# Performance work log

Measured on AMD Instinct MI355X. Metric: run time of the kernel, lower is better.

## Reference

```python
import jax, jax.numpy as jnp
import numpy as np

DEPTH = 4
DIM = 1024
HEADS = 16
DIM_HEAD = 64
INNER = HEADS * DIM_HEAD  # 1024
MLP = 4096
CTX = 768
SCALE = DIM_HEAD ** -0.5
EPS = 1e-5


def setup_inputs() -> dict:
    key = jax.random.key(0)
    ks = jax.random.split(key, 12)
    def rn(k, shape, s=0.02):
        return jax.random.normal(k, shape, jnp.float32) * s
    return {
        "x": jax.random.normal(ks[0], (2, 2048, DIM), jnp.float32),
        "context": jax.random.normal(ks[1], (2, 1024, CTX), jnp.float32),
        "ln1_g": jnp.ones((DEPTH, DIM), jnp.float32),
        "ln1_b": jnp.zeros((DEPTH, DIM), jnp.float32),
        "w_qkv": rn(ks[2], (DEPTH, DIM, 3 * INNER)),
        "w_sa_o": rn(ks[3], (DEPTH, INNER, DIM)),
        "b_sa_o": jnp.zeros((DEPTH, DIM), jnp.float32),
        "ln2_g": jnp.ones((DEPTH, DIM), jnp.float32),
        "ln2_b": jnp.zeros((DEPTH, DIM), jnp.float32),
        "w_q": rn(ks[4], (DEPTH, DIM, INNER)),
        "w_kv": rn(ks[5], (DEPTH, CTX, 2 * INNER)),
        "w_ca_o": rn(ks[6], (DEPTH, INNER, DIM)),
        "b_ca_o": jnp.zeros((DEPTH, DIM), jnp.float32),
        "ln3_g": jnp.ones((DEPTH, DIM), jnp.float32),
        "ln3_b": jnp.zeros((DEPTH, DIM), jnp.float32),
        "w_ff1": rn(ks[7], (DEPTH, DIM, MLP)),
        "b_ff1": jnp.zeros((DEPTH, MLP), jnp.float32),
        "w_ff2": rn(ks[8], (DEPTH, MLP, DIM)),
        "b_ff2": jnp.zeros((DEPTH, DIM), jnp.float32),
    }


def _ln(x, g, b):
    mu = jnp.mean(x, axis=-1, keepdims=True)
    var = jnp.mean(jnp.square(x - mu), axis=-1, keepdims=True)
    return (x - mu) * jax.lax.rsqrt(var + EPS) * g + b


def _heads(t):
    # [b, n, h*d] -> [b, h, n, d]
    b, n, _ = t.shape
    return t.reshape(b, n, HEADS, DIM_HEAD).transpose(0, 2, 1, 3)


def _mha(q, k, v):
    # q,k,v: [b, h, n, d]; naive matmul-softmax-matmul, same math as the torch code
    attn = jax.nn.softmax(jnp.einsum('bhqd,bhkd->bhqk', q, k) * SCALE, axis=-1)
    out = jnp.einsum('bhqk,bhkd->bhqd', attn, v)
    b, h, n, d = out.shape
    return out.transpose(0, 2, 1, 3).reshape(b, n, h * d)


def reference(x, context, ln1_g, ln1_b, w_qkv, w_sa_o, b_sa_o,
              ln2_g, ln2_b, w_q, w_kv, w_ca_o, b_ca_o,
              ln3_g, ln3_b, w_ff1, b_ff1, w_ff2, b_ff2):
    for i in range(DEPTH):
        # self-attention
        h = _ln(x, ln1_g[i], ln1_b[i])
        qkv = h @ w_qkv[i]
        q, k, v = jnp.split(qkv, 3, axis=-1)
        sa = _mha(_heads(q), _heads(k), _heads(v)) @ w_sa_o[i] + b_sa_o[i]
        x = sa + x
        # cross-attention
        h = _ln(x, ln2_g[i], ln2_b[i])
        q = h @ w_q[i]
        kv = context @ w_kv[i]
        k, v = jnp.split(kv, 2, axis=-1)
        ca = _mha(_heads(q), _heads(k), _heads(v)) @ w_ca_o[i] + b_ca_o[i]
        x = ca + x
        # feed-forward (exact GELU, matching torch nn.GELU default)
        h = _ln(x, ln3_g[i], ln3_b[i])
        ff = jax.nn.gelu(h @ w_ff1[i] + b_ff1[i], approximate=False) @ w_ff2[i] + b_ff2[i]
        x = ff + x
    return x
```

## Files before the change

### kernel.cpp

```cpp
#include <hip/hip_runtime.h>
#include <hip/hip_bf16.h>
#include <math.h>

typedef __bf16 bf16_t;
typedef __bf16 bf16x8 __attribute__((ext_vector_type(8)));
typedef __bf16 bf16x4 __attribute__((ext_vector_type(4)));
typedef float f32x4 __attribute__((ext_vector_type(4)));
typedef unsigned short u16;
typedef unsigned int u32;
typedef u16 u16x8 __attribute__((ext_vector_type(8)));

#define NDEPTH 4
#define DIM 1024
#define NHEADS 16
#define MLP_DIM 4096
#define CTXD 768
#define NTOK 4096
#define NCTX 2048
#define ATT_SCALE 0.125f

__device__ inline void gload_lds16(const void* g, void* l) {
  __builtin_amdgcn_global_load_lds(
      (const __attribute__((address_space(1))) void*)g,
      (__attribute__((address_space(3))) void*)l, 16, 0, 0);
}

__device__ inline u32 packbf2(float a, float b) {
  union { bf16_t h[2]; u32 w; } u;
  u.h[0] = (bf16_t)a; u.h[1] = (bf16_t)b;
  return u.w;
}

template<int EPI>
__global__ __launch_bounds__(256) void gemm_bf16(
    const bf16_t* __restrict__ A, const bf16_t* __restrict__ Bt,
    const float* __restrict__ bias, const float* __restrict__ res,
    void* __restrict__ outp, int M, int N, int K)
{
  __shared__ bf16_t As[2][128 * 32];
  __shared__ bf16_t Bs[2][128 * 32];
  const int tid = threadIdx.x, lane = tid & 63, wave = tid >> 6;
  const int bx = blockIdx.x, by = blockIdx.y;
  const int wr = wave >> 1, wc = wave & 1;
  const int l15 = lane & 15, l4 = lane >> 4;

  const bf16_t* Ag = A + (size_t)by * 128 * K;
  const bf16_t* Bg = Bt + (size_t)bx * 128 * K;

  f32x4 acc[4][4] = {};

  auto stage = [&](int buf, int k0) {
#pragma unroll
    for (int r = 0; r < 2; ++r) {
      int cbase = r * 256 + wave * 64;
      int c = cbase + lane;
      int row = c >> 2, off = (c & 3) * 8;
      gload_lds16(Ag + (size_t)row * K + k0 + off, &As[buf][(size_t)cbase * 8]);
      gload_lds16(Bg + (size_t)row * K + k0 + off, &Bs[buf][(size_t)cbase * 8]);
    }
  };

  const int nk = K >> 5;
  stage(0, 0);
  __syncthreads();
  for (int t = 0; t < nk; ++t) {
    const int cur = t & 1;
    if (t + 1 < nk) stage(cur ^ 1, (t + 1) << 5);
    bf16x8 af[4], bfr[4];
#pragma unroll
    for (int mi = 0; mi < 4; ++mi)
      af[mi] = *(const bf16x8*)&As[cur][(wr * 64 + mi * 16 + l15) * 32 + l4 * 8];
#pragma unroll
    for (int ni = 0; ni < 4; ++ni)
      bfr[ni] = *(const bf16x8*)&Bs[cur][(wc * 64 + ni * 16 + l15) * 32 + l4 * 8];
#pragma unroll
    for (int mi = 0; mi < 4; ++mi)
#pragma unroll
      for (int ni = 0; ni < 4; ++ni)
        acc[mi][ni] = __builtin_amdgcn_mfma_f32_16x16x32_bf16(af[mi], bfr[ni], acc[mi][ni], 0, 0, 0);
    __syncthreads();
  }

  const int r0 = by * 128 + wr * 64, c0 = bx * 128 + wc * 64;
#pragma unroll
  for (int ni = 0; ni < 4; ++ni) {
    int col = c0 + ni * 16 + l15;
    float bv = (EPI == 0) ? 0.f : bias[col];
#pragma unroll
    for (int mi = 0; mi < 4; ++mi) {
#pragma unroll
      for (int r = 0; r < 4; ++r) {
        int row = r0 + mi * 16 + l4 * 4 + r;
        float v = acc[mi][ni][r] + bv;
        size_t idx = (size_t)row * N + col;
        if (EPI == 3) {
          ((float*)outp)[idx] = v + res[idx];
        } else if (EPI == 2) {
          float gv = 0.5f * v * (1.f + erff(v * 0.70710678118f));
          ((bf16_t*)outp)[idx] = (bf16_t)gv;
        } else {
          ((bf16_t*)outp)[idx] = (bf16_t)v;
        }
      }
    }
  }
}

__global__ __launch_bounds__(512) void attn_fwd(
    const bf16_t* __restrict__ Q, int qs,
    const bf16_t* __restrict__ K, const bf16_t* __restrict__ V, int kvs,
    bf16_t* __restrict__ O, int os, int nq, int nk)
{
  __shared__ bf16_t Ks[2][64][72];
  __shared__ bf16_t Vt[2][64][72];

  const int tid = threadIdx.x, lane = tid & 63, wv = tid >> 6;
  const int l15 = lane & 15, l4 = lane >> 4;
  const int h = blockIdx.y, bz = blockIdx.z;
  const size_t qrow0 = (size_t)bz * nq + (size_t)blockIdx.x * 128;
  const bf16_t* Qb = Q + (qrow0 + wv * 16) * qs + h * 64;
  const bf16_t* Kb = K + (size_t)bz * nk * kvs + h * 64;
  const bf16_t* Vb = V + (size_t)bz * nk * kvs + h * 64;
  bf16_t* Ob = O + (qrow0 + wv * 16) * os + h * 64;

  bf16x8 qa[2];
#pragma unroll
  for (int ks = 0; ks < 2; ++ks)
    qa[ks] = *(const bf16x8*)(Qb + (size_t)l15 * qs + ks * 32 + l4 * 8);

  const int krow = tid >> 3, kcol = (tid & 7) * 8;

  u16x8 kreg, vreg;
  auto load_tile = [&](int kt) {
    kreg = *(const u16x8*)(Kb + (size_t)(kt * 64 + krow) * kvs + kcol);
    u16x8 t;
#pragma unroll
    for (int i = 0; i < 8; ++i)
      t[i] = *(const u16*)(Vb + (size_t)(kt * 64 + wv * 8 + i) * kvs + lane);
    vreg = t;
  };
  auto store_tile = [&](int buf) {
    *(u16x8*)&Ks[buf][krow][kcol] = kreg;
    *(u16x8*)&Vt[buf][lane][wv * 8] = vreg;
  };

  float m_run = -1e30f, l_run = 0.f;
  f32x4 acc[4] = {};

  const int ntiles = nk >> 6;
  load_tile(0);
  store_tile(0);
  __syncthreads();

  for (int kt = 0; kt < ntiles; ++kt) {
    const int cur = kt & 1;
    const bool pre = (kt + 1 < ntiles);
    if (pre) load_tile(kt + 1);

    f32x4 s[4] = {};
#pragma unroll
    for (int ks = 0; ks < 2; ++ks)
#pragma unroll
      for (int f = 0; f < 4; ++f) {
        bf16x8 kf = *(const bf16x8*)&Ks[cur][f * 16 + l15][ks * 32 + l4 * 8];
        s[f] = __builtin_amdgcn_mfma_f32_16x16x32_bf16(kf, qa[ks], s[f], 0, 0, 0);
      }

    float smax = s[0][0];
#pragma unroll
    for (int f = 0; f < 4; ++f)
#pragma unroll
      for (int r = 0; r < 4; ++r) smax = fmaxf(smax, s[f][r]);
    smax = fmaxf(smax, __shfl_xor(smax, 16));
    smax = fmaxf(smax, __shfl_xor(smax, 32));
    smax *= ATT_SCALE;
    const float mn = fmaxf(m_run, smax);
    const float esc = __expf(m_run - mn);
    m_run = mn;

    float p[4][4], psum = 0.f;
#pragma unroll
    for (int f = 0; f < 4; ++f)
#pragma unroll
      for (int r = 0; r < 4; ++r) {
        float pv = __expf(s[f][r] * ATT_SCALE - mn);
        p[f][r] = pv;
        psum += pv;
      }
    psum += __shfl_xor(psum, 16);
    psum += __shfl_xor(psum, 32);
    l_run = l_run * esc + psum;

#pragma unroll
    for (int r = 0; r < 4; ++r) {
      float eq = __shfl(esc, (l4 << 4) + (l4 << 2) + r);
#pragma unroll
      for (int d0 = 0; d0 < 4; ++d0) acc[d0][r] *= eq;
    }

    u32 pk[4][2];
#pragma unroll
    for (int f = 0; f < 4; ++f)
#pragma unroll
      for (int hh = 0; hh < 2; ++hh)
        pk[f][hh] = packbf2(p[f][2 * hh], p[f][2 * hh + 1]);

    bf16x8 pa[2];
#pragma unroll
    for (int ks = 0; ks < 2; ++ks) {
      union { u32 w[4]; bf16x8 v; } pu;
#pragma unroll
      for (int jj = 0; jj < 4; ++jj) {
        int src = l15 + ((((l4 << 1) + (jj >> 1)) & 3) << 4);
        u32 a = (u32)__shfl((int)pk[ks * 2 + 0][jj & 1], src);
        u32 b = (u32)__shfl((int)pk[ks * 2 + 1][jj & 1], src);
        pu.w[jj] = (l4 & 2) ? b : a;
      }
      pa[ks] = pu.v;
    }

#pragma unroll
    for (int ks = 0; ks < 2; ++ks)
#pragma unroll
      for (int d0 = 0; d0 < 4; ++d0) {
        bf16x8 vb = *(const bf16x8*)&Vt[cur][d0 * 16 + l15][ks * 32 + l4 * 8];
        acc[d0] = __builtin_amdgcn_mfma_f32_16x16x32_bf16(pa[ks], vb, acc[d0], 0, 0, 0);
      }

    if (pre) store_tile(cur ^ 1);
    __syncthreads();
  }

#pragma unroll
  for (int r = 0; r < 4; ++r) {
    float lq = __shfl(l_run, (l4 << 4) + (l4 << 2) + r);
    float inv = 1.f / lq;
#pragma unroll
    for (int d0 = 0; d0 < 4; ++d0)
      Ob[(size_t)(l4 * 4 + r) * os + d0 * 16 + l15] = (bf16_t)(acc[d0][r] * inv);
  }
}

__global__ __launch_bounds__(256) void layernorm_f32_bf16(
    const float* __restrict__ x, const float* __restrict__ g, const float* __restrict__ b,
    bf16_t* __restrict__ out)
{
  const int row = blockIdx.x, tid = threadIdx.x;
  const float4 v = ((const float4*)(x + (size_t)row * 1024))[tid];
  float s = v.x + v.y + v.z + v.w;
  float s2 = v.x * v.x + v.y * v.y + v.z * v.z + v.w * v.w;
#pragma unroll
  for (int off = 32; off > 0; off >>= 1) {
    s += __shfl_down(s, off);
    s2 += __shfl_down(s2, off);
  }
  __shared__ float ps[4], ps2[4];
  const int lane = tid & 63, wave = tid >> 6;
  if (lane == 0) { ps[wave] = s; ps2[wave] = s2; }
  __syncthreads();
  s = ps[0] + ps[1] + ps[2] + ps[3];
  s2 = ps2[0] + ps2[1] + ps2[2] + ps2[3];
  const float mu = s * (1.f / 1024.f);
  const float var = s2 * (1.f / 1024.f) - mu * mu;
  const float rstd = rsqrtf(var + 1e-5f);
  const float4 gv = ((const float4*)g)[tid];
  const float4 bv = ((const float4*)b)[tid];
  bf16x4 o;
  o[0] = (bf16_t)((v.x - mu) * rstd * gv.x + bv.x);
  o[1] = (bf16_t)((v.y - mu) * rstd * gv.y + bv.y);
  o[2] = (bf16_t)((v.z - mu) * rstd * gv.z + bv.z);
  o[3] = (bf16_t)((v.w - mu) * rstd * gv.w + bv.w);
  *(bf16x4*)(out + (size_t)row * 1024 + tid * 4) = o;
}

__global__ void transpose_to_bf16(const float* __restrict__ src, bf16_t* __restrict__ dst, int K, int N)
{
  __shared__ float tile[32][33];
  const size_t loff = (size_t)blockIdx.z * K * N;
  src += loff; dst += loff;
  const int k0 = blockIdx.y * 32, n0 = blockIdx.x * 32;
  const int tx = threadIdx.x, ty = threadIdx.y;
#pragma unroll
  for (int i = ty; i < 32; i += 8)
    tile[i][tx] = src[(size_t)(k0 + i) * N + n0 + tx];
  __syncthreads();
#pragma unroll
  for (int i = ty; i < 32; i += 8)
    dst[(size_t)(n0 + i) * K + k0 + tx] = (bf16_t)tile[tx][i];
}

__global__ void f32_to_bf16(const float* __restrict__ src, bf16_t* __restrict__ dst, int n4)
{
  int i = blockIdx.x * blockDim.x + threadIdx.x;
  if (i < n4) {
    float4 v = ((const float4*)src)[i];
    bf16x4 o;
    o[0] = (bf16_t)v.x; o[1] = (bf16_t)v.y; o[2] = (bf16_t)v.z; o[3] = (bf16_t)v.w;
    ((bf16x4*)dst)[i] = o;
  }
}

__global__ void copy_f32(const float* __restrict__ src, float* __restrict__ dst, int n4)
{
  int i = blockIdx.x * blockDim.x + threadIdx.x;
  if (i < n4) ((float4*)dst)[i] = ((const float4*)src)[i];
}

extern "C" void kernel_launch(void* const* d_in, const int* in_sizes, int n_in,
                              void* d_out, int out_size, void* d_ws, size_t ws_size,
                              hipStream_t stream)
{
  const float* x      = (const float*)d_in[0];
  const float* ctx    = (const float*)d_in[1];
  const float* ln1_g  = (const float*)d_in[2];
  const float* ln1_b  = (const float*)d_in[3];
  const float* w_qkv  = (const float*)d_in[4];
  const float* w_sa_o = (const float*)d_in[5];
  const float* b_sa_o = (const float*)d_in[6];
  const float* ln2_g  = (const float*)d_in[7];
  const float* ln2_b  = (const float*)d_in[8];
  const float* w_q    = (const float*)d_in[9];
  const float* w_kv   = (const float*)d_in[10];
  const float* w_ca_o = (const float*)d_in[11];
  const float* b_ca_o = (const float*)d_in[12];
  const float* ln3_g  = (const float*)d_in[13];
  const float* ln3_b  = (const float*)d_in[14];
  const float* w_ff1  = (const float*)d_in[15];
  const float* b_ff1  = (const float*)d_in[16];
  const float* w_ff2  = (const float*)d_in[17];
  const float* b_ff2  = (const float*)d_in[18];

  char* p = (char*)d_ws;
  auto alloc = [&](size_t bytes) { char* r = p; p += (bytes + 255) & ~(size_t)255; return r; };
  bf16_t* wqkv_t = (bf16_t*)alloc((size_t)NDEPTH * 3072 * 1024 * 2);
  bf16_t* wsao_t = (bf16_t*)alloc((size_t)NDEPTH * 1024 * 1024 * 2);
  bf16_t* wq_t   = (bf16_t*)alloc((size_t)NDEPTH * 1024 * 1024 * 2);
  bf16_t* wkv_t  = (bf16_t*)alloc((size_t)NDEPTH * 2048 * 768 * 2);
  bf16_t* wcao_t = (bf16_t*)alloc((size_t)NDEPTH * 1024 * 1024 * 2);
  bf16_t* wff1_t = (bf16_t*)alloc((size_t)NDEPTH * 4096 * 1024 * 2);
  bf16_t* wff2_t = (bf16_t*)alloc((size_t)NDEPTH * 1024 * 4096 * 2);
  bf16_t* ctxb   = (bf16_t*)alloc((size_t)NCTX * CTXD * 2);
  float*  xbuf   = (float*)alloc((size_t)NTOK * DIM * 4);
  bf16_t* lnbuf  = (bf16_t*)alloc((size_t)NTOK * DIM * 2);
  bf16_t* bigbuf = (bf16_t*)alloc((size_t)NTOK * 4096 * 2);
  bf16_t* qbuf   = (bf16_t*)alloc((size_t)NTOK * DIM * 2);
  bf16_t* kvbuf  = (bf16_t*)alloc((size_t)NCTX * 2048 * 2);
  if ((size_t)(p - (char*)d_ws) > ws_size) return;

  dim3 tb(32, 8);
  transpose_to_bf16<<<dim3(3072 / 32, 1024 / 32, NDEPTH), tb, 0, stream>>>(w_qkv, wqkv_t, 1024, 3072);
  transpose_to_bf16<<<dim3(1024 / 32, 1024 / 32, NDEPTH), tb, 0, stream>>>(w_sa_o, wsao_t, 1024, 1024);
  transpose_to_bf16<<<dim3(1024 / 32, 1024 / 32, NDEPTH), tb, 0, stream>>>(w_q, wq_t, 1024, 1024);
  transpose_to_bf16<<<dim3(2048 / 32, 768 / 32, NDEPTH), tb, 0, stream>>>(w_kv, wkv_t, 768, 2048);
  transpose_to_bf16<<<dim3(1024 / 32, 1024 / 32, NDEPTH), tb, 0, stream>>>(w_ca_o, wcao_t, 1024, 1024);
  transpose_to_bf16<<<dim3(4096 / 32, 1024 / 32, NDEPTH), tb, 0, stream>>>(w_ff1, wff1_t, 1024, 4096);
  transpose_to_bf16<<<dim3(1024 / 32, 4096 / 32, NDEPTH), tb, 0, stream>>>(w_ff2, wff2_t, 4096, 1024);
  f32_to_bf16<<<(NCTX * CTXD / 4 + 255) / 256, 256, 0, stream>>>(ctx, ctxb, NCTX * CTXD / 4);
  copy_f32<<<(NTOK * DIM / 4 + 255) / 256, 256, 0, stream>>>(x, xbuf, NTOK * DIM / 4);

  for (int i = 0; i < NDEPTH; ++i) {
    layernorm_f32_bf16<<<NTOK, 256, 0, stream>>>(xbuf, ln1_g + i * DIM, ln1_b + i * DIM, lnbuf);
    gemm_bf16<0><<<dim3(3072 / 128, NTOK / 128), 256, 0, stream>>>(
        lnbuf, wqkv_t + (size_t)i * 3072 * 1024, nullptr, nullptr, bigbuf, NTOK, 3072, 1024);
    attn_fwd<<<dim3(2048 / 128, NHEADS, 2), 512, 0, stream>>>(
        bigbuf, 3072, bigbuf + 1024, bigbuf + 2048, 3072, lnbuf, 1024, 2048, 2048);
    gemm_bf16<3><<<dim3(1024 / 128, NTOK / 128), 256, 0, stream>>>(
        lnbuf, wsao_t + (size_t)i * 1024 * 1024, b_sa_o + i * DIM, xbuf, xbuf, NTOK, 1024, 1024);
    layernorm_f32_bf16<<<NTOK, 256, 0, stream>>>(xbuf, ln2_g + i * DIM, ln2_b + i * DIM, lnbuf);
    gemm_bf16<0><<<dim3(1024 / 128, NTOK / 128), 256, 0, stream>>>(
        lnbuf, wq_t + (size_t)i * 1024 * 1024, nullptr, nullptr, qbuf, NTOK, 1024, 1024);
    gemm_bf16<0><<<dim3(2048 / 128, NCTX / 128), 256, 0, stream>>>(
        ctxb, wkv_t + (size_t)i * 2048 * 768, nullptr, nullptr, kvbuf, NCTX, 2048, 768);
    attn_fwd<<<dim3(2048 / 128, NHEADS, 2), 512, 0, stream>>>(
        qbuf, 1024, kvbuf, kvbuf + 1024, 2048, lnbuf, 1024, 2048, 1024);
    gemm_bf16<3><<<dim3(1024 / 128, NTOK / 128), 256, 0, stream>>>(
        lnbuf, wcao_t + (size_t)i * 1024 * 1024, b_ca_o + i * DIM, xbuf, xbuf, NTOK, 1024, 1024);
    layernorm_f32_bf16<<<NTOK, 256, 0, stream>>>(xbuf, ln3_g + i * DIM, ln3_b + i * DIM, lnbuf);
    gemm_bf16<2><<<dim3(4096 / 128, NTOK / 128), 256, 0, stream>>>(
        lnbuf, wff1_t + (size_t)i * 4096 * 1024, b_ff1 + i * MLP_DIM, nullptr, bigbuf, NTOK, 4096, 1024);
    gemm_bf16<3><<<dim3(1024 / 128, NTOK / 128), 256, 0, stream>>>(
        bigbuf, wff2_t + (size_t)i * 1024 * 4096, b_ff2 + i * DIM, xbuf, xbuf, NTOK, 1024, 4096);
  }
  copy_f32<<<(NTOK * DIM / 4 + 255) / 256, 256, 0, stream>>>(xbuf, (float*)d_out, NTOK * DIM / 4);
}
```

Before: 1.933 ms.

## Use 8-wave GEMM blocks with triple-buffered LDS and explicit vmcnt waits

The bf16 GEMM goes from 4 to 8 waves per 128x128 tile, so each wave computes 64x32 instead of 64x64. LDS staging moves from double to triple buffering with a prefetch depth of two, and __syncthreads is replaced by explicit s_waitcnt vmcnt plus s_barrier so global loads can stay in flight across iterations. The aim is more latency hiding and better overlap of loads with MFMA work. In exchange, LDS use rises and each wave does less MFMA work per fragment load, and the hand-tuned vmcnt counts rely on every thread issuing exactly two loads per stage.

```diff
diff --git a/kernel.cpp b/kernel.cpp
--- a/kernel.cpp
+++ b/kernel.cpp
@@ -32,58 +32,67 @@
 }
 
 template<int EPI>
-__global__ __launch_bounds__(256) void gemm_bf16(
+__global__ __launch_bounds__(512) void gemm_bf16(
     const bf16_t* __restrict__ A, const bf16_t* __restrict__ Bt,
     const float* __restrict__ bias, const float* __restrict__ res,
     void* __restrict__ outp, int M, int N, int K)
 {
-  __shared__ bf16_t As[2][128 * 32];
-  __shared__ bf16_t Bs[2][128 * 32];
+  __shared__ alignas(16) bf16_t As[3][128 * 32];
+  __shared__ alignas(16) bf16_t Bs[3][128 * 32];
   const int tid = threadIdx.x, lane = tid & 63, wave = tid >> 6;
   const int bx = blockIdx.x, by = blockIdx.y;
-  const int wr = wave >> 1, wc = wave & 1;
+  const int wr = wave >> 2, wc = wave & 3;
   const int l15 = lane & 15, l4 = lane >> 4;
 
   const bf16_t* Ag = A + (size_t)by * 128 * K;
   const bf16_t* Bg = Bt + (size_t)bx * 128 * K;
 
-  f32x4 acc[4][4] = {};
-
+  f32x4 acc[4][2] = {};
+
+  const int srow = tid >> 2, soff = (tid & 3) * 8;
   auto stage = [&](int buf, int k0) {
-#pragma unroll
-    for (int r = 0; r < 2; ++r) {
-      int cbase = r * 256 + wave * 64;
-      int c = cbase + lane;
-      int row = c >> 2, off = (c & 3) * 8;
-      gload_lds16(Ag + (size_t)row * K + k0 + off, &As[buf][(size_t)cbase * 8]);
-      gload_lds16(Bg + (size_t)row * K + k0 + off, &Bs[buf][(size_t)cbase * 8]);
-    }
+    gload_lds16(Ag + (size_t)srow * K + k0 + soff, &As[buf][(size_t)tid * 8]);
+    gload_lds16(Bg + (size_t)srow * K + k0 + soff, &Bs[buf][(size_t)tid * 8]);
   };
 
   const int nk = K >> 5;
   stage(0, 0);
-  __syncthreads();
+  stage(1, 32);
+  asm volatile("s_waitcnt vmcnt(2)" ::: "memory");
+  __builtin_amdgcn_s_barrier();
+  __builtin_amdgcn_sched_barrier(0);
+
   for (int t = 0; t < nk; ++t) {
-    const int cur = t & 1;
-    if (t + 1 < nk) stage(cur ^ 1, (t + 1) << 5);
-    bf16x8 af[4], bfr[4];
+    const int cur = t % 3;
+    if (t + 2 < nk) stage((t + 2) % 3, (t + 2) << 5);
+
+    bf16x8 af[4], bfr[2];
 #pragma unroll
     for (int mi = 0; mi < 4; ++mi)
       af[mi] = *(const bf16x8*)&As[cur][(wr * 64 + mi * 16 + l15) * 32 + l4 * 8];
 #pragma unroll
-    for (int ni = 0; ni < 4; ++ni)
-      bfr[ni] = *(const bf16x8*)&Bs[cur][(wc * 64 + ni * 16 + l15) * 32 + l4 * 8];
+    for (int ni = 0; ni < 2; ++ni)
+      bfr[ni] = *(const bf16x8*)&Bs[cur][(wc * 32 + ni * 16 + l15) * 32 + l4 * 8];
 #pragma unroll
     for (int mi = 0; mi < 4; ++mi)
 #pragma unroll
-      for (int ni = 0; ni < 4; ++ni)
+      for (int ni = 0; ni < 2; ++ni)
         acc[mi][ni] = __builtin_amdgcn_mfma_f32_16x16x32_bf16(af[mi], bfr[ni], acc[mi][ni], 0, 0, 0);
-    __syncthreads();
-  }
-
-  const int r0 = by * 128 + wr * 64, c0 = bx * 128 + wc * 64;
-#pragma unroll
-  for (int ni = 0; ni < 4; ++ni) {
+
+    if (t + 2 < nk) {
+      asm volatile("s_waitcnt vmcnt(2)" ::: "memory");
+    } else if (t + 1 < nk) {
+      asm volatile("s_waitcnt vmcnt(0)" ::: "memory");
+    } else {
+      break;
+    }
+    __builtin_amdgcn_s_barrier();
+    __builtin_amdgcn_sched_barrier(0);
+  }
+
+  const int r0 = by * 128 + wr * 64, c0 = bx * 128 + wc * 32;
+#pragma unroll
+  for (int ni = 0; ni < 2; ++ni) {
     int col = c0 + ni * 16 + l15;
     float bv = (EPI == 0) ? 0.f : bias[col];
 #pragma unroll
@@ -360,25 +369,25 @@
 
   for (int i = 0; i < NDEPTH; ++i) {
     layernorm_f32_bf16<<<NTOK, 256, 0, stream>>>(xbuf, ln1_g + i * DIM, ln1_b + i * DIM, lnbuf);
-    gemm_bf16<0><<<dim3(3072 / 128, NTOK / 128), 256, 0, stream>>>(
+    gemm_bf16<0><<<dim3(3072 / 128, NTOK / 128), 512, 0, stream>>>(
         lnbuf, wqkv_t + (size_t)i * 3072 * 1024, nullptr, nullptr, bigbuf, NTOK, 3072, 1024);
     attn_fwd<<<dim3(2048 / 128, NHEADS, 2), 512, 0, stream>>>(
         bigbuf, 3072, bigbuf + 1024, bigbuf + 2048, 3072, lnbuf, 1024, 2048, 2048);
-    gemm_bf16<3><<<dim3(1024 / 128, NTOK / 128), 256, 0, stream>>>(
+    gemm_bf16<3><<<dim3(1024 / 128, NTOK / 128), 512, 0, stream>>>(
         lnbuf, wsao_t + (size_t)i * 1024 * 1024, b_sa_o + i * DIM, xbuf, xbuf, NTOK, 1024, 1024);
     layernorm_f32_bf16<<<NTOK, 256, 0, stream>>>(xbuf, ln2_g + i * DIM, ln2_b + i * DIM, lnbuf);
-    gemm_bf16<0><<<dim3(1024 / 128, NTOK / 128), 256, 0, stream>>>(
+    gemm_bf16<0><<<dim3(1024 / 128, NTOK / 128), 512, 0, stream>>>(
         lnbuf, wq_t + (size_t)i * 1024 * 1024, nullptr, nullptr, qbuf, NTOK, 1024, 1024);
-    gemm_bf16<0><<<dim3(2048 / 128, NCTX / 128), 256, 0, stream>>>(
+    gemm_bf16<0><<<dim3(2048 / 128, NCTX / 128), 512, 0, stream>>>(
         ctxb, wkv_t + (size_t)i * 2048 * 768, nullptr, nullptr, kvbuf, NCTX, 2048, 768);
     attn_fwd<<<dim3(2048 / 128, NHEADS, 2), 512, 0, stream>>>(
         qbuf, 1024, kvbuf, kvbuf + 1024, 2048, lnbuf, 1024, 2048, 1024);
-    gemm_bf16<3><<<dim3(1024 / 128, NTOK / 128), 256, 0, stream>>>(
+    gemm_bf16<3><<<dim3(1024 / 128, NTOK / 128), 512, 0, stream>>>(
         lnbuf, wcao_t + (size_t)i * 1024 * 1024, b_ca_o + i * DIM, xbuf, xbuf, NTOK, 1024, 1024);
     layernorm_f32_bf16<<<NTOK, 256, 0, stream>>>(xbuf, ln3_g + i * DIM, ln3_b + i * DIM, lnbuf);
-    gemm_bf16<2><<<dim3(4096 / 128, NTOK / 128), 256, 0, stream>>>(
+    gemm_bf16<2><<<dim3(4096 / 128, NTOK / 128), 512, 0, stream>>>(
         lnbuf, wff1_t + (size_t)i * 4096 * 1024, b_ff1 + i * MLP_DIM, nullptr, bigbuf, NTOK, 4096, 1024);
-    gemm_bf16<3><<<dim3(1024 / 128, NTOK / 128), 256, 0, stream>>>(
+    gemm_bf16<3><<<dim3(1024 / 128, NTOK / 128), 512, 0, stream>>>(
         bigbuf, wff2_t + (size_t)i * 1024 * 4096, b_ff2 + i * DIM, xbuf, xbuf, NTOK, 1024, 4096);
   }
   copy_f32<<<(NTOK * DIM / 4 + 255) / 256, 256, 0, stream>>>(xbuf, (float*)d_out, NTOK * DIM / 4);
```

New measurement: 1.864 ms. 3.6% less time.
